# Kernel tuning notes

Hardware: AMD Instinct MI355X
Metric: run time of the kernel (lower is better)

## Reference

```python
import jax, jax.numpy as jnp
import numpy as np

HEADS = 12
DIM_HEAD = 64
SCALE = DIM_HEAD ** -0.5


def setup_inputs() -> dict:
    key = jax.random.key(0)
    ks = jax.random.split(key, 5)
    b, n, dim = 16, 1024, 768
    inner = HEADS * DIM_HEAD  # 768
    x = jax.random.normal(ks[0], (b, n, dim), dtype=jnp.float32)
    w_qv = jax.random.normal(ks[1], (dim, 2 * inner), dtype=jnp.float32) * (dim ** -0.5)
    ext_k = jax.random.normal(ks[2], (1, HEADS, n, DIM_HEAD), dtype=jnp.float32)
    ext_bias = jax.random.normal(ks[3], (1, HEADS, n, n), dtype=jnp.float32)
    w_out = jax.random.normal(ks[4], (inner, dim), dtype=jnp.float32) * (inner ** -0.5)
    b_out = jnp.zeros((dim,), dtype=jnp.float32)
    return {"x": x, "w_qv": w_qv, "ext_k": ext_k, "ext_bias": ext_bias,
            "w_out": w_out, "b_out": b_out}


def reference(x, w_qv, ext_k, ext_bias, w_out, b_out):
    b, n, _ = x.shape
    qv = x @ w_qv                                   # [b, n, 2*inner]
    q, v = jnp.split(qv, 2, axis=-1)
    # b n (h d) -> b h n d
    q = q.reshape(b, n, HEADS, DIM_HEAD).transpose(0, 2, 1, 3)
    v = v.reshape(b, n, HEADS, DIM_HEAD).transpose(0, 2, 1, 3)
    # dots = (q @ ext_k^T + ext_bias) * scale       # [b, h, n, n]
    dots = (jnp.einsum('bhnd,ohmd->bhnm', q, ext_k) + ext_bias) * SCALE
    attn = jax.nn.softmax(dots, axis=-1)
    out = jnp.einsum('bhnm,bhmd->bhnd', attn, v)    # [b, h, n, d]
    out = out.transpose(0, 2, 1, 3).reshape(b, n, HEADS * DIM_HEAD)
    return out @ w_out + b_out
```

## Files before the change

kernel.cpp:

```cpp
#include <hip/hip_runtime.h>
#include <hip/hip_bf16.h>
#include <stdint.h>

typedef __bf16 bf16;
typedef short  s16x8 __attribute__((ext_vector_type(8)));
typedef float  f32x4 __attribute__((ext_vector_type(4)));

#define NHEADS  12
#define QKSCALE 0.125f

__device__ __forceinline__ void gload_lds16(const void* g, void* l) {
  __builtin_amdgcn_global_load_lds(
      (__attribute__((address_space(1))) void*)(g),
      (__attribute__((address_space(3))) void*)(l), 16, 0, 0);
}

__device__ __forceinline__ short bf16bits(float f) {
  union { bf16 h; short s; } u;
  u.h = (bf16)f;
  return u.s;
}
__device__ __forceinline__ float bfu2f(unsigned short u) {
  union { unsigned int i; float f; } c;
  c.i = ((unsigned int)u) << 16;
  return c.f;
}

__global__ __launch_bounds__(256) void cast4_kernel(const float* __restrict__ in,
                                                    bf16* __restrict__ out,
                                                    int n4, float scale) {
  int i = blockIdx.x * 256 + threadIdx.x;
  if (i >= n4) return;
  float4 v = ((const float4*)in)[i];
  union { bf16 h[4]; uint64_t u; } o;
  o.h[0] = (bf16)(v.x * scale);
  o.h[1] = (bf16)(v.y * scale);
  o.h[2] = (bf16)(v.z * scale);
  o.h[3] = (bf16)(v.w * scale);
  ((uint64_t*)out)[i] = o.u;
}

__global__ __launch_bounds__(256) void castT_tiled(const float* __restrict__ in,
                                                   bf16* __restrict__ out,
                                                   int R, int C) {
  __shared__ float tile[32][33];
  const int nbx = C >> 5;
  const int bx = blockIdx.x % nbx, by = blockIdx.x / nbx;
  const int tx = threadIdx.x & 31, ty = threadIdx.x >> 5;
  const int r0 = by << 5, c0 = bx << 5;
#pragma unroll
  for (int i = 0; i < 4; ++i)
    tile[ty + i * 8][tx] = in[(size_t)(r0 + ty + i * 8) * C + c0 + tx];
  __syncthreads();
#pragma unroll
  for (int i = 0; i < 4; ++i)
    out[(size_t)(c0 + ty + i * 8) * R + r0 + tx] = (bf16)tile[tx][ty + i * 8];
}

template <int EPI>
__global__ __launch_bounds__(256) void gemm128(const bf16* __restrict__ A,
                                               const bf16* __restrict__ BT,
                                               int M, int N, int K,
                                               bf16* __restrict__ outQ,
                                               bf16* __restrict__ outVT,
                                               float* __restrict__ outC,
                                               const float* __restrict__ bias) {
  __shared__ char sA[8192];
  __shared__ char sB[8192];
  const int nb = N >> 7;
  const int bx = blockIdx.x % nb, by = blockIdx.x / nb;
  const int brow = by << 7, bcol = bx << 7;
  const int t = threadIdx.x;
  const int w = t >> 6, l = t & 63;
  const int wr = w >> 1, wc = w & 1;
  const int lr = l & 15, lg = l >> 4;

  const f32x4 fz = {0.f, 0.f, 0.f, 0.f};
  f32x4 acc[4][4];
#pragma unroll
  for (int m = 0; m < 4; ++m)
#pragma unroll
    for (int n = 0; n < 4; ++n) acc[m][n] = fz;

  const int nk = K >> 5;
  for (int kt = 0; kt < nk; ++kt) {
#pragma unroll
    for (int i = 0; i < 2; ++i) {
      int chunk = ((i * 4 + w) << 6) + l;
      int rrow = chunk >> 2, rc = chunk & 3;
      gload_lds16(A + (size_t)(brow + rrow) * K + (kt << 5) + (rc << 3),
                  sA + ((i * 4 + w) << 10));
      gload_lds16(BT + (size_t)(bcol + rrow) * K + (kt << 5) + (rc << 3),
                  sB + ((i * 4 + w) << 10));
    }
    __syncthreads();
    s16x8 af[4], bfr[4];
#pragma unroll
    for (int m = 0; m < 4; ++m)
      af[m] = *(const s16x8*)(sA + ((wr << 6) + (m << 4) + lr) * 64 + (lg << 4));
#pragma unroll
    for (int n = 0; n < 4; ++n)
      bfr[n] = *(const s16x8*)(sB + ((wc << 6) + (n << 4) + lr) * 64 + (lg << 4));
#pragma unroll
    for (int m = 0; m < 4; ++m)
#pragma unroll
      for (int n = 0; n < 4; ++n)
        acc[m][n] = __builtin_amdgcn_mfma_f32_16x16x32_bf16(af[m], bfr[n], acc[m][n], 0, 0, 0);
    __syncthreads();
  }

  if (EPI == 0) {
#pragma unroll
    for (int n = 0; n < 4; ++n) {
      int gcol = bcol + (wc << 6) + (n << 4) + lr;
      if (gcol < 768) {
        int h = gcol >> 6, d = gcol & 63;
#pragma unroll
        for (int m = 0; m < 4; ++m) {
          int growb = brow + (wr << 6) + (m << 4) + (lg << 2);
#pragma unroll
          for (int r = 0; r < 4; ++r) {
            int grow = growb + r;
            int b = grow >> 10, nr = grow & 1023;
            outQ[(((size_t)(b * NHEADS + h) << 10) + nr) * 64 + d] =
                (bf16)(acc[m][n][r] * QKSCALE);
          }
        }
      } else {
        int c2 = gcol - 768;
        int h = c2 >> 6, d = c2 & 63;
#pragma unroll
        for (int m = 0; m < 4; ++m) {
          int growb = brow + (wr << 6) + (m << 4) + (lg << 2);
          int b = growb >> 10, nr0 = growb & 1023;
          ushort4 pk;
          pk.x = (unsigned short)bf16bits(acc[m][n][0]);
          pk.y = (unsigned short)bf16bits(acc[m][n][1]);
          pk.z = (unsigned short)bf16bits(acc[m][n][2]);
          pk.w = (unsigned short)bf16bits(acc[m][n][3]);
          *(ushort4*)(outVT + ((((size_t)(b * NHEADS + h) << 6) + d) << 10) + nr0) = pk;
        }
      }
    }
  } else {
#pragma unroll
    for (int n = 0; n < 4; ++n) {
      int gcol = bcol + (wc << 6) + (n << 4) + lr;
      float bv = bias[gcol];
#pragma unroll
      for (int m = 0; m < 4; ++m) {
        int growb = brow + (wr << 6) + (m << 4) + (lg << 2);
#pragma unroll
        for (int r = 0; r < 4; ++r)
          outC[(size_t)(growb + r) * N + gcol] = acc[m][n][r] + bv;
      }
    }
  }
}

__global__ __launch_bounds__(256) void attn_kernel(const bf16* __restrict__ Q,
                                                   const bf16* __restrict__ VT,
                                                   const bf16* __restrict__ Kx,
                                                   const bf16* __restrict__ Bias,
                                                   bf16* __restrict__ O) {
  __shared__ char sK[2][8192];
  __shared__ char sVT[2][8192];
  __shared__ char sP[4][2048];

  const int blk = blockIdx.x;
  const int b  = blk & 15;
  const int qb = (blk >> 4) & 15;
  const int h  = blk >> 8;
  const int bh = b * NHEADS + h;
  const int t = threadIdx.x, w = t >> 6, l = t & 63;
  const int lr = l & 15, lg = l >> 4;
  const int q0 = (qb << 6) + (w << 4);
  const size_t qvbase = (size_t)bh << 10;

  s16x8 qf[2];
#pragma unroll
  for (int kf = 0; kf < 2; ++kf)
    qf[kf] = *(const s16x8*)(Q + ((qvbase + q0 + lr) << 6) + (kf << 5) + (lg << 3));

  const f32x4 fz = {0.f, 0.f, 0.f, 0.f};
  f32x4 acc_o[4];
#pragma unroll
  for (int of = 0; of < 4; ++of) acc_o[of] = fz;
  float lsum = 0.f;

  const bf16* Kh = Kx + ((size_t)h << 16);
  const bf16* Brow = Bias + ((size_t)((h << 10) + q0 + lr)) * 1024;
  const bf16* Vth = VT + (qvbase << 6);

#define STAGE_K(kt_, buf_)                                                  \
  {                                                                         \
    _Pragma("unroll") for (int i = 0; i < 2; ++i) {                         \
      int rowloc = ((i * 4 + w) << 3) + (l >> 3);                           \
      int chunk = (l & 7) ^ (rowloc & 7);                                   \
      gload_lds16(Kh + ((((kt_) << 6) + rowloc) << 6) + (chunk << 3),       \
                  sK[buf_] + ((i * 4 + w) << 10));                          \
    }                                                                       \
  }
#define STAGE_VT(kt_, buf_)                                                 \
  {                                                                         \
    _Pragma("unroll") for (int i = 0; i < 2; ++i) {                         \
      int rowloc = ((i * 4 + w) << 3) + (l >> 3);          \
      int chunk = (l & 7) ^ (rowloc & 7);                                   \
      gload_lds16(Vth + ((size_t)rowloc << 10) + ((kt_) << 6) + (chunk << 3), \
                  sVT[buf_] + ((i * 4 + w) << 10));                         \
    }                                                                       \
  }

  STAGE_K(0, 0);
  STAGE_VT(0, 0);
  ushort4 bu_cur[4];
#pragma unroll
  for (int cf = 0; cf < 4; ++cf)
    bu_cur[cf] = *(const ushort4*)(Brow + (cf << 4) + (lg << 2));
  __syncthreads();

  for (int kt = 0; kt < 16; ++kt) {
    const int cur = kt & 1, nxt = cur ^ 1;
    if (kt < 15) {
      STAGE_K(kt + 1, nxt);
      STAGE_VT(kt + 1, nxt);
    }

    float bfv[4][4];
#pragma unroll
    for (int cf = 0; cf < 4; ++cf) {
      bfv[cf][0] = bfu2f(bu_cur[cf].x);
      bfv[cf][1] = bfu2f(bu_cur[cf].y);
      bfv[cf][2] = bfu2f(bu_cur[cf].z);
      bfv[cf][3] = bfu2f(bu_cur[cf].w);
    }

    f32x4 s[4];
    __builtin_amdgcn_s_setprio(1);
#pragma unroll
    for (int cf = 0; cf < 4; ++cf) {
      int kvloc = (cf << 4) + lr;
      f32x4 z = {bfv[cf][0], bfv[cf][1], bfv[cf][2], bfv[cf][3]};
#pragma unroll
      for (int kf = 0; kf < 2; ++kf) {
        int chunk = ((kf << 2) + lg) ^ (kvloc & 7);
        s16x8 kb8 = *(const s16x8*)(sK[cur] + (kvloc << 7) + (chunk << 4));
        z = __builtin_amdgcn_mfma_f32_16x16x32_bf16(kb8, qf[kf], z, 0, 0, 0);
      }
      s[cf] = z;
    }
    __builtin_amdgcn_s_setprio(0);

    float psum = 0.f;
#pragma unroll
    for (int cf = 0; cf < 4; ++cf)
#pragma unroll
      for (int r = 0; r < 4; ++r) {
        float p = __expf(s[cf][r]);
        s[cf][r] = p;
        psum += p;
      }
    lsum += psum;

#pragma unroll
    for (int cf = 0; cf < 4; ++cf) {
      ushort4 pk;
      pk.x = (unsigned short)bf16bits(s[cf][0]);
      pk.y = (unsigned short)bf16bits(s[cf][1]);
      pk.z = (unsigned short)bf16bits(s[cf][2]);
      pk.w = (unsigned short)bf16bits(s[cf][3]);
      int kvbyte = (cf << 5) + (lg << 3);
      int off = (lr << 7) + ((((kvbyte >> 4) ^ (lr & 7)) << 4) | (kvbyte & 15));
      *(ushort4*)(sP[w] + off) = pk;
    }
    s16x8 pa[2];
#pragma unroll
    for (int kf2 = 0; kf2 < 2; ++kf2) {
      int chunk = ((kf2 << 2) + lg) ^ (lr & 7);
      pa[kf2] = *(const s16x8*)(sP[w] + (lr << 7) + (chunk << 4));
    }

    if (kt < 15) {
#pragma unroll
      for (int cf = 0; cf < 4; ++cf)
        bu_cur[cf] = *(const ushort4*)(Brow + ((kt + 1) << 6) + (cf << 4) + (lg << 2));
    }

    __builtin_amdgcn_s_setprio(1);
#pragma unroll
    for (int of = 0; of < 4; ++of) {
      int d = (of << 4) + lr;
#pragma unroll
      for (int kf2 = 0; kf2 < 2; ++kf2) {
        int chunk = ((kf2 << 2) + lg) ^ (d & 7);
        s16x8 vbf = *(const s16x8*)(sVT[cur] + (d << 7) + (chunk << 4));
        acc_o[of] = __builtin_amdgcn_mfma_f32_16x16x32_bf16(pa[kf2], vbf, acc_o[of], 0, 0, 0);
      }
    }
    __builtin_amdgcn_s_setprio(0);

    __syncthreads();
  }

  lsum += __shfl_xor(lsum, 16);
  lsum += __shfl_xor(lsum, 32);
  float inv[4];
#pragma unroll
  for (int r = 0; r < 4; ++r)
    inv[r] = 1.0f / __shfl(lsum, (lg << 4) + (lg << 2) + r);
#pragma unroll
  for (int of = 0; of < 4; ++of)
#pragma unroll
    for (int r = 0; r < 4; ++r) {
      int qrow = q0 + (lg << 2) + r;
      size_t off = ((size_t)((b << 10) + qrow)) * 768 + (h << 6) + (of << 4) + lr;
      O[off] = (bf16)(acc_o[of][r] * inv[r]);
    }
#undef STAGE_K
#undef STAGE_VT
}

extern "C" void kernel_launch(void* const* d_in, const int* in_sizes, int n_in,
                              void* d_out, int out_size, void* d_ws, size_t ws_size,
                              hipStream_t stream) {
  const float* x        = (const float*)d_in[0];
  const float* w_qv     = (const float*)d_in[1];
  const float* ext_k    = (const float*)d_in[2];
  const float* ext_bias = (const float*)d_in[3];
  const float* w_out    = (const float*)d_in[4];
  const float* b_out    = (const float*)d_in[5];
  float* out = (float*)d_out;

  char* ws = (char*)d_ws;
  bf16* xb    = (bf16*)(ws);
  bf16* wqvT  = (bf16*)(ws + 25165824);
  bf16* kb    = (bf16*)(ws + 27525120);
  bf16* wobT  = (bf16*)(ws + 29097984);
  bf16* biasb = (bf16*)(ws + 30277632);
  bf16* qws   = (bf16*)(ws + 55443456);
  bf16* vtws  = (bf16*)(ws + 80609280);
  bf16* attout = xb;

  cast4_kernel<<<12288, 256, 0, stream>>>(x, xb, 3145728, 1.0f);
  cast4_kernel<<<12288, 256, 0, stream>>>(ext_bias, biasb, 3145728, QKSCALE);
  cast4_kernel<<<768, 256, 0, stream>>>(ext_k, kb, 196608, 1.0f);
  castT_tiled<<<1152, 256, 0, stream>>>(w_qv, wqvT, 768, 1536);
  castT_tiled<<<576, 256, 0, stream>>>(w_out, wobT, 768, 768);

  gemm128<0><<<1536, 256, 0, stream>>>(xb, wqvT, 16384, 1536, 768, qws, vtws, nullptr, nullptr);
  attn_kernel<<<3072, 256, 0, stream>>>(qws, vtws, kb, biasb, attout);
  gemm128<1><<<768, 256, 0, stream>>>(attout, wobT, 16384, 768, 768, nullptr, nullptr, out, b_out);
}
```

Baseline: 387.4 us.

## Double-buffer GEMM loads, double attention query tile, remap blocks across XCDs

The GEMM now double-buffers its A/B shared-memory tiles, prefetching the next K slice while MFMAs run on the current one, and raises wave priority around the MFMA block. The attention kernel now gives each wave 32 query rows in two groups of 16, so every K/V tile loaded into shared memory serves twice as many queries, and the grid is halved. Both kernels remap block indices with an 8-way XCD-aware swizzle to improve L2 locality. The cost is higher register and LDS use per block, which may lower occupancy.

Result: no change. 381.7 us (-1.5%).

```diff
diff --git a/kernel.cpp b/kernel.cpp
--- a/kernel.cpp
+++ b/kernel.cpp
@@ -65,10 +65,13 @@
                                                bf16* __restrict__ outVT,
                                                float* __restrict__ outC,
                                                const float* __restrict__ bias) {
-  __shared__ char sA[8192];
-  __shared__ char sB[8192];
+  __shared__ char sA[2][8192];
+  __shared__ char sB[2][8192];
+  const int cpx = gridDim.x >> 3;
+  const int orig = blockIdx.x;
+  const int blk = (orig & 7) * cpx + (orig >> 3);
   const int nb = N >> 7;
-  const int bx = blockIdx.x % nb, by = blockIdx.x / nb;
+  const int bx = blk % nb, by = blk / nb;
   const int brow = by << 7, bcol = bx << 7;
   const int t = threadIdx.x;
   const int w = t >> 6, l = t & 63;
@@ -82,32 +85,41 @@
 #pragma unroll
     for (int n = 0; n < 4; ++n) acc[m][n] = fz;
 
+#define G_STAGE(kt_, buf_)                                                     \
+  {                                                                            \
+    _Pragma("unroll") for (int i = 0; i < 2; ++i) {                            \
+      int chunk = ((i * 4 + w) << 6) + l;                                      \
+      int rrow = chunk >> 2, rc = chunk & 3;                                   \
+      gload_lds16(A + (size_t)(brow + rrow) * K + ((kt_) << 5) + (rc << 3),    \
+                  sA[buf_] + ((i * 4 + w) << 10));                             \
+      gload_lds16(BT + (size_t)(bcol + rrow) * K + ((kt_) << 5) + (rc << 3),   \
+                  sB[buf_] + ((i * 4 + w) << 10));                             \
+    }                                                                          \
+  }
+
   const int nk = K >> 5;
+  G_STAGE(0, 0);
+  __syncthreads();
   for (int kt = 0; kt < nk; ++kt) {
-#pragma unroll
-    for (int i = 0; i < 2; ++i) {
-      int chunk = ((i * 4 + w) << 6) + l;
-      int rrow = chunk >> 2, rc = chunk & 3;
-      gload_lds16(A + (size_t)(brow + rrow) * K + (kt << 5) + (rc << 3),
-                  sA + ((i * 4 + w) << 10));
-      gload_lds16(BT + (size_t)(bcol + rrow) * K + (kt << 5) + (rc << 3),
-                  sB + ((i * 4 + w) << 10));
-    }
-    __syncthreads();
+    const int cur = kt & 1, nxt = cur ^ 1;
+    if (kt + 1 < nk) G_STAGE(kt + 1, nxt);
     s16x8 af[4], bfr[4];
 #pragma unroll
     for (int m = 0; m < 4; ++m)
-      af[m] = *(const s16x8*)(sA + ((wr << 6) + (m << 4) + lr) * 64 + (lg << 4));
+      af[m] = *(const s16x8*)(sA[cur] + ((wr << 6) + (m << 4) + lr) * 64 + (lg << 4));
 #pragma unroll
     for (int n = 0; n < 4; ++n)
-      bfr[n] = *(const s16x8*)(sB + ((wc << 6) + (n << 4) + lr) * 64 + (lg << 4));
+      bfr[n] = *(const s16x8*)(sB[cur] + ((wc << 6) + (n << 4) + lr) * 64 + (lg << 4));
+    __builtin_amdgcn_s_setprio(1);
 #pragma unroll
     for (int m = 0; m < 4; ++m)
 #pragma unroll
       for (int n = 0; n < 4; ++n)
         acc[m][n] = __builtin_amdgcn_mfma_f32_16x16x32_bf16(af[m], bfr[n], acc[m][n], 0, 0, 0);
+    __builtin_amdgcn_s_setprio(0);
     __syncthreads();
   }
+#undef G_STAGE
 
   if (EPI == 0) {
 #pragma unroll
@@ -165,31 +177,40 @@
                                                    bf16* __restrict__ O) {
   __shared__ char sK[2][8192];
   __shared__ char sVT[2][8192];
-  __shared__ char sP[4][2048];
-
-  const int blk = blockIdx.x;
+  __shared__ char sP[4][4096];
+
+  const int cpx = gridDim.x >> 3;
+  const int orig = blockIdx.x;
+  const int blk = (orig & 7) * cpx + (orig >> 3);
+
   const int b  = blk & 15;
-  const int qb = (blk >> 4) & 15;
-  const int h  = blk >> 8;
+  const int qb = (blk >> 4) & 7;
+  const int h  = blk >> 7;
   const int bh = b * NHEADS + h;
   const int t = threadIdx.x, w = t >> 6, l = t & 63;
   const int lr = l & 15, lg = l >> 4;
-  const int q0 = (qb << 6) + (w << 4);
+  const int q0 = (qb << 7) + (w << 5);
   const size_t qvbase = (size_t)bh << 10;
 
-  s16x8 qf[2];
-#pragma unroll
-  for (int kf = 0; kf < 2; ++kf)
-    qf[kf] = *(const s16x8*)(Q + ((qvbase + q0 + lr) << 6) + (kf << 5) + (lg << 3));
+  s16x8 qf[2][2];
+#pragma unroll
+  for (int qg = 0; qg < 2; ++qg)
+#pragma unroll
+    for (int kf = 0; kf < 2; ++kf)
+      qf[qg][kf] = *(const s16x8*)(Q + ((qvbase + q0 + (qg << 4) + lr) << 6) +
+                                   (kf << 5) + (lg << 3));
 
   const f32x4 fz = {0.f, 0.f, 0.f, 0.f};
-  f32x4 acc_o[4];
-#pragma unroll
-  for (int of = 0; of < 4; ++of) acc_o[of] = fz;
-  float lsum = 0.f;
+  f32x4 acc_o[2][4];
+#pragma unroll
+  for (int qg = 0; qg < 2; ++qg)
+#pragma unroll
+    for (int of = 0; of < 4; ++of) acc_o[qg][of] = fz;
+  float lsum[2] = {0.f, 0.f};
 
   const bf16* Kh = Kx + ((size_t)h << 16);
-  const bf16* Brow = Bias + ((size_t)((h << 10) + q0 + lr)) * 1024;
+  const bf16* Brow0 = Bias + ((size_t)((h << 10) + q0 + lr)) * 1024;
+  const bf16* Brow1 = Brow0 + (16 << 10);
   const bf16* Vth = VT + (qvbase << 6);
 
 #define STAGE_K(kt_, buf_)                                                  \
@@ -213,10 +234,12 @@
 
   STAGE_K(0, 0);
   STAGE_VT(0, 0);
-  ushort4 bu_cur[4];
-#pragma unroll
-  for (int cf = 0; cf < 4; ++cf)
-    bu_cur[cf] = *(const ushort4*)(Brow + (cf << 4) + (lg << 2));
+  ushort4 bu[2][4];
+#pragma unroll
+  for (int cf = 0; cf < 4; ++cf) {
+    bu[0][cf] = *(const ushort4*)(Brow0 + (cf << 4) + (lg << 2));
+    bu[1][cf] = *(const ushort4*)(Brow1 + (cf << 4) + (lg << 2));
+  }
   __syncthreads();
 
   for (int kt = 0; kt < 16; ++kt) {
@@ -226,64 +249,73 @@
       STAGE_VT(kt + 1, nxt);
     }
 
-    float bfv[4][4];
-#pragma unroll
-    for (int cf = 0; cf < 4; ++cf) {
-      bfv[cf][0] = bfu2f(bu_cur[cf].x);
-      bfv[cf][1] = bfu2f(bu_cur[cf].y);
-      bfv[cf][2] = bfu2f(bu_cur[cf].z);
-      bfv[cf][3] = bfu2f(bu_cur[cf].w);
-    }
-
-    f32x4 s[4];
+    f32x4 s[2][4];
+#pragma unroll
+    for (int qg = 0; qg < 2; ++qg)
+#pragma unroll
+      for (int cf = 0; cf < 4; ++cf) {
+        s[qg][cf][0] = bfu2f(bu[qg][cf].x);
+        s[qg][cf][1] = bfu2f(bu[qg][cf].y);
+        s[qg][cf][2] = bfu2f(bu[qg][cf].z);
+        s[qg][cf][3] = bfu2f(bu[qg][cf].w);
+      }
     __builtin_amdgcn_s_setprio(1);
 #pragma unroll
     for (int cf = 0; cf < 4; ++cf) {
       int kvloc = (cf << 4) + lr;
-      f32x4 z = {bfv[cf][0], bfv[cf][1], bfv[cf][2], bfv[cf][3]};
 #pragma unroll
       for (int kf = 0; kf < 2; ++kf) {
         int chunk = ((kf << 2) + lg) ^ (kvloc & 7);
         s16x8 kb8 = *(const s16x8*)(sK[cur] + (kvloc << 7) + (chunk << 4));
-        z = __builtin_amdgcn_mfma_f32_16x16x32_bf16(kb8, qf[kf], z, 0, 0, 0);
-      }
-      s[cf] = z;
+        s[0][cf] = __builtin_amdgcn_mfma_f32_16x16x32_bf16(kb8, qf[0][kf], s[0][cf], 0, 0, 0);
+        s[1][cf] = __builtin_amdgcn_mfma_f32_16x16x32_bf16(kb8, qf[1][kf], s[1][cf], 0, 0, 0);
+      }
     }
     __builtin_amdgcn_s_setprio(0);
 
-    float psum = 0.f;
-#pragma unroll
-    for (int cf = 0; cf < 4; ++cf)
-#pragma unroll
-      for (int r = 0; r < 4; ++r) {
-        float p = __expf(s[cf][r]);
-        s[cf][r] = p;
-        psum += p;
-      }
-    lsum += psum;
-
-#pragma unroll
-    for (int cf = 0; cf < 4; ++cf) {
-      ushort4 pk;
-      pk.x = (unsigned short)bf16bits(s[cf][0]);
-      pk.y = (unsigned short)bf16bits(s[cf][1]);
-      pk.z = (unsigned short)bf16bits(s[cf][2]);
-      pk.w = (unsigned short)bf16bits(s[cf][3]);
-      int kvbyte = (cf << 5) + (lg << 3);
-      int off = (lr << 7) + ((((kvbyte >> 4) ^ (lr & 7)) << 4) | (kvbyte & 15));
-      *(ushort4*)(sP[w] + off) = pk;
-    }
-    s16x8 pa[2];
-#pragma unroll
-    for (int kf2 = 0; kf2 < 2; ++kf2) {
-      int chunk = ((kf2 << 2) + lg) ^ (lr & 7);
-      pa[kf2] = *(const s16x8*)(sP[w] + (lr << 7) + (chunk << 4));
-    }
+#pragma unroll
+    for (int qg = 0; qg < 2; ++qg) {
+      float psum = 0.f;
+#pragma unroll
+      for (int cf = 0; cf < 4; ++cf)
+#pragma unroll
+        for (int r = 0; r < 4; ++r) {
+          float p = __expf(s[qg][cf][r]);
+          s[qg][cf][r] = p;
+          psum += p;
+        }
+      lsum[qg] += psum;
+    }
+
+#pragma unroll
+    for (int qg = 0; qg < 2; ++qg)
+#pragma unroll
+      for (int cf = 0; cf < 4; ++cf) {
+        ushort4 pk;
+        pk.x = (unsigned short)bf16bits(s[qg][cf][0]);
+        pk.y = (unsigned short)bf16bits(s[qg][cf][1]);
+        pk.z = (unsigned short)bf16bits(s[qg][cf][2]);
+        pk.w = (unsigned short)bf16bits(s[qg][cf][3]);
+        int kvbyte = (cf << 5) + (lg << 3);
+        int off = (qg << 11) + (lr << 7) +
+                  ((((kvbyte >> 4) ^ (lr & 7)) << 4) | (kvbyte & 15));
+        *(ushort4*)(sP[w] + off) = pk;
+      }
+    s16x8 pa[2][2];
+#pragma unroll
+    for (int qg = 0; qg < 2; ++qg)
+#pragma unroll
+      for (int kf2 = 0; kf2 < 2; ++kf2) {
+        int chunk = ((kf2 << 2) + lg) ^ (lr & 7);
+        pa[qg][kf2] = *(const s16x8*)(sP[w] + (qg << 11) + (lr << 7) + (chunk << 4));
+      }
 
     if (kt < 15) {
 #pragma unroll
-      for (int cf = 0; cf < 4; ++cf)
-        bu_cur[cf] = *(const ushort4*)(Brow + ((kt + 1) << 6) + (cf << 4) + (lg << 2));
+      for (int cf = 0; cf < 4; ++cf) {
+        bu[0][cf] = *(const ushort4*)(Brow0 + ((kt + 1) << 6) + (cf << 4) + (lg << 2));
+        bu[1][cf] = *(const ushort4*)(Brow1 + ((kt + 1) << 6) + (cf << 4) + (lg << 2));
+      }
     }
 
     __builtin_amdgcn_s_setprio(1);
@@ -294,7 +326,8 @@
       for (int kf2 = 0; kf2 < 2; ++kf2) {
         int chunk = ((kf2 << 2) + lg) ^ (d & 7);
         s16x8 vbf = *(const s16x8*)(sVT[cur] + (d << 7) + (chunk << 4));
-        acc_o[of] = __builtin_amdgcn_mfma_f32_16x16x32_bf16(pa[kf2], vbf, acc_o[of], 0, 0, 0);
+        acc_o[0][of] = __builtin_amdgcn_mfma_f32_16x16x32_bf16(pa[0][kf2], vbf, acc_o[0][of], 0, 0, 0);
+        acc_o[1][of] = __builtin_amdgcn_mfma_f32_16x16x32_bf16(pa[1][kf2], vbf, acc_o[1][of], 0, 0, 0);
       }
     }
     __builtin_amdgcn_s_setprio(0);
@@ -302,20 +335,25 @@
     __syncthreads();
   }
 
-  lsum += __shfl_xor(lsum, 16);
-  lsum += __shfl_xor(lsum, 32);
-  float inv[4];
-#pragma unroll
-  for (int r = 0; r < 4; ++r)
-    inv[r] = 1.0f / __shfl(lsum, (lg << 4) + (lg << 2) + r);
-#pragma unroll
-  for (int of = 0; of < 4; ++of)
-#pragma unroll
-    for (int r = 0; r < 4; ++r) {
-      int qrow = q0 + (lg << 2) + r;
-      size_t off = ((size_t)((b << 10) + qrow)) * 768 + (h << 6) + (of << 4) + lr;
-      O[off] = (bf16)(acc_o[of][r] * inv[r]);
-    }
+  const int bb = b;
+#pragma unroll
+  for (int qg = 0; qg < 2; ++qg) {
+    float ls = lsum[qg];
+    ls += __shfl_xor(ls, 16);
+    ls += __shfl_xor(ls, 32);
+    float inv[4];
+#pragma unroll
+    for (int r = 0; r < 4; ++r)
+      inv[r] = 1.0f / __shfl(ls, (lg << 4) + (lg << 2) + r);
+#pragma unroll
+    for (int of = 0; of < 4; ++of)
+#pragma unroll
+      for (int r = 0; r < 4; ++r) {
+        int qrow = q0 + (qg << 4) + (lg << 2) + r;
+        size_t off = ((size_t)((bb << 10) + qrow)) * 768 + (h << 6) + (of << 4) + lr;
+        O[off] = (bf16)(acc_o[qg][of][r] * inv[r]);
+      }
+  }
 #undef STAGE_K
 #undef STAGE_VT
 }
@@ -348,6 +386,6 @@
   castT_tiled<<<576, 256, 0, stream>>>(w_out, wobT, 768, 768);
 
   gemm128<0><<<1536, 256, 0, stream>>>(xb, wqvT, 16384, 1536, 768, qws, vtws, nullptr, nullptr);
-  attn_kernel<<<3072, 256, 0, stream>>>(qws, vtws, kb, biasb, attout);
+  attn_kernel<<<1536, 256, 0, stream>>>(qws, vtws, kb, biasb, attout);
   gemm128<1><<<768, 256, 0, stream>>>(attout, wobT, 16384, 768, 768, nullptr, nullptr, out, b_out);
 }
```
